# Optimization experiments

Hardware: AMD Instinct MI355X
Metric: run time of the kernel (lower is better)

The kernel has to match this reference:

```python
import jax, jax.numpy as jnp
import numpy as np

B, C, T = 2, 2, 4
N_SRC = 49152   # npix at level 6 (12 * 4^6)
N_TGT = 12288   # npix at level 5 (12 * 4^5)
D = 128


def setup_inputs() -> dict:
    key = jax.random.key(0)
    k1, k2, k3, k4 = jax.random.split(key, 4)
    x = jax.random.normal(k1, (B, C, T, N_SRC, D), dtype=jnp.float32)
    parent_map = jax.random.randint(k2, (N_SRC,), 0, N_TGT)
    W = jax.random.normal(k3, (D, D), dtype=jnp.float32) * 0.05  # Conv1d kernel_size=1 weight [out,in]
    b = jax.random.normal(k4, (D,), dtype=jnp.float32) * 0.05    # Conv1d bias
    return {"x": x, "parent_map": parent_map, "W": W, "b": b}


def reference(x, parent_map, W, b):
    # HEALPix downsample: scatter-add mean pooling over parent_map, then 1x1 conv.
    Bs, Cs, Ts, N, Dd = x.shape
    # flatten (b c t) and put pixel axis first for segment_sum: [N, BCT, D]
    x2 = x.reshape(Bs * Cs * Ts, N, Dd).transpose(1, 0, 2)
    sums = jax.ops.segment_sum(x2, parent_map, num_segments=N_TGT)          # [N_TGT, BCT, D]
    cnt = jax.ops.segment_sum(jnp.ones((N,), x.dtype), parent_map, num_segments=N_TGT)
    mean = sums / jnp.clip(cnt, 1e-6)[:, None, None]
    # 1x1 Conv1d over channel dim D: y = W @ mean + b
    out = jnp.einsum('mbd,ed->mbe', mean, W) + b                            # [N_TGT, BCT, D]
    return out.transpose(1, 0, 2).reshape(Bs, Cs, Ts, N_TGT, Dd)
```

## Files before the change

### kernel.cpp

```cpp
#include <hip/hip_runtime.h>
#include <stdint.h>

#define NSRC 49152
#define NTGT 12288
#define DIM  128
#define MPER 8
#define ROWS (MPER*16)
#define CAP  32
#define OSTR 132

using short8  = __attribute__((ext_vector_type(8))) short;
using short4v = __attribute__((ext_vector_type(4))) short;
using bf16x8  = __attribute__((ext_vector_type(8))) __bf16;
using f32x4   = __attribute__((ext_vector_type(4))) float;

__device__ __forceinline__ short f2bf(float f){
  unsigned int u = __float_as_uint(f);
  return (short)((u + 0x7fffu + ((u >> 16) & 1u)) >> 16);
}

__global__ void k_setup(const int* __restrict__ pm,
                        int* __restrict__ counts, int* __restrict__ child,
                        const float* __restrict__ W, short* __restrict__ Wt){
  const int b = blockIdx.x;
  if (b < 192){
    int i = b * 256 + threadIdx.x;
    int p = pm[i];
    int pos = atomicAdd(&counts[p], 1);
    if (pos < CAP) child[p * CAP + pos] = i;
  } else {
    int t  = (b - 192) * 256 + threadIdx.x;
    int e  = t & 127;
    int kk = t >> 7;
    const float4* src = (const float4*)(W + (size_t)e * DIM + kk * 8);
    float4 u = src[0], v = src[1];
    short8 h;
    h[0]=f2bf(u.x); h[1]=f2bf(u.y); h[2]=f2bf(u.z); h[3]=f2bf(u.w);
    h[4]=f2bf(v.x); h[5]=f2bf(v.y); h[6]=f2bf(v.z); h[7]=f2bf(v.w);
    *reinterpret_cast<short8*>(Wt + ((size_t)kk * 128 + e) * 8) = h;
  }
}

__global__ __launch_bounds__(256, 4) void k_fused(
    const float* __restrict__ x, const short* __restrict__ Wt,
    const float* __restrict__ bias,
    const int* __restrict__ counts, const int* __restrict__ child,
    float* __restrict__ out)
{
  __shared__ __align__(16) char smem[64 * OSTR * 4];
  short* s_mean = (short*)smem;
  float* s_out  = (float*)smem;
  const int tid = threadIdx.x;
  const int m0  = blockIdx.x * MPER;

  {
    const int o = tid & 7;
    #pragma unroll
    for (int it = 0; it < 4; ++it){
      const int r   = it * 32 + (tid >> 3);
      const int m   = m0 + (r >> 4);
      const int bct = r & 15;
      int cnt = counts[m]; cnt = (cnt > CAP) ? CAP : cnt;
      const int* cl = child + (size_t)m * CAP;
      const float* rowb = x + (size_t)bct * NSRC * DIM;
      float4 acc[4];
      #pragma unroll
      for (int s = 0; s < 4; ++s) acc[s] = make_float4(0.f, 0.f, 0.f, 0.f);
      int c = 0;
      for (; c + 1 < cnt; c += 2){
        const int n0 = cl[c], n1 = cl[c + 1];
        const float4* p0 = (const float4*)(rowb + (size_t)n0 * DIM) + o;
        const float4* p1 = (const float4*)(rowb + (size_t)n1 * DIM) + o;
        float4 v0[4], v1[4];
        #pragma unroll
        for (int s = 0; s < 4; ++s) v0[s] = p0[s * 8];
        #pragma unroll
        for (int s = 0; s < 4; ++s) v1[s] = p1[s * 8];
        #pragma unroll
        for (int s = 0; s < 4; ++s){
          acc[s].x += v0[s].x + v1[s].x; acc[s].y += v0[s].y + v1[s].y;
          acc[s].z += v0[s].z + v1[s].z; acc[s].w += v0[s].w + v1[s].w;
        }
      }
      if (c < cnt){
        const int n0 = cl[c];
        const float4* p0 = (const float4*)(rowb + (size_t)n0 * DIM) + o;
        #pragma unroll
        for (int s = 0; s < 4; ++s){
          float4 v = p0[s * 8];
          acc[s].x += v.x; acc[s].y += v.y; acc[s].z += v.z; acc[s].w += v.w;
        }
      }
      const float inv = (cnt > 0) ? (1.0f / (float)cnt) : 0.0f;
      const int rsw = (r & 7) << 3;
      #pragma unroll
      for (int s = 0; s < 4; ++s){
        const int col = s * 32 + o * 4;
        short4v h;
        h[0] = f2bf(acc[s].x * inv); h[1] = f2bf(acc[s].y * inv);
        h[2] = f2bf(acc[s].z * inv); h[3] = f2bf(acc[s].w * inv);
        *reinterpret_cast<short4v*>(&s_mean[r * DIM + (col ^ rsw)]) = h;
      }
    }
  }

  __syncthreads();

  const int w  = tid >> 6;
  const int l  = tid & 63;
  const int lr = l & 15;
  const int kg = l >> 4;
  f32x4 acc[2][8];
  #pragma unroll
  for (int i = 0; i < 2; ++i)
    #pragma unroll
    for (int n = 0; n < 8; ++n) acc[i][n] = (f32x4){0.f, 0.f, 0.f, 0.f};

  #pragma unroll 1
  for (int ks = 0; ks < 4; ++ks){
    const int k = ks * 32 + kg * 8;
    bf16x8 af[2];
    #pragma unroll
    for (int i = 0; i < 2; ++i){
      const int row = w * 32 + i * 16 + lr;
      af[i] = *reinterpret_cast<bf16x8*>(&s_mean[row * DIM + (k ^ ((row & 7) << 3))]);
    }
    const short* wp = Wt + ((size_t)(ks * 4 + kg) * 128 + lr) * 8;
    #pragma unroll
    for (int n = 0; n < 8; ++n){
      bf16x8 bfr = *reinterpret_cast<const bf16x8*>(wp + n * 128);
      acc[0][n] = __builtin_amdgcn_mfma_f32_16x16x32_bf16(af[0], bfr, acc[0][n], 0, 0, 0);
      acc[1][n] = __builtin_amdgcn_mfma_f32_16x16x32_bf16(af[1], bfr, acc[1][n], 0, 0, 0);
    }
  }

  float bv[8];
  #pragma unroll
  for (int n = 0; n < 8; ++n) bv[n] = bias[n * 16 + lr];

  #pragma unroll
  for (int round = 0; round < 2; ++round){
    __syncthreads();
    if ((w >> 1) == round){
      #pragma unroll
      for (int i = 0; i < 2; ++i)
        #pragma unroll
        for (int j = 0; j < 4; ++j){
          const int grl = (w & 1) * 32 + i * 16 + (l >> 4) * 4 + j;
          #pragma unroll
          for (int n = 0; n < 8; ++n)
            s_out[grl * OSTR + n * 16 + lr] = acc[i][n][j] + bv[n];
        }
    }
    __syncthreads();
    #pragma unroll
    for (int r2 = 0; r2 < 4; ++r2){
      const int bct = w * 4 + r2;
      #pragma unroll
      for (int it2 = 0; it2 < 2; ++it2){
        const int f  = it2 * 64 + l;
        const int mi = f >> 5, d4 = f & 31;
        f32x4 v = *reinterpret_cast<f32x4*>(&s_out[(mi * 16 + bct) * OSTR + d4 * 4]);
        float* gp = out + ((size_t)bct * NTGT + m0 + round * 4 + mi) * DIM + d4 * 4;
        __builtin_nontemporal_store(v, reinterpret_cast<f32x4*>(gp));
      }
    }
  }
}

extern "C" void kernel_launch(void* const* d_in, const int* in_sizes, int n_in,
                              void* d_out, int out_size, void* d_ws, size_t ws_size,
                              hipStream_t stream) {
  const float* x    = (const float*)d_in[0];
  const int*   pm   = (const int*)  d_in[1];
  const float* W    = (const float*)d_in[2];
  const float* bias = (const float*)d_in[3];
  float* out = (float*)d_out;

  int*   counts = (int*)d_ws;
  int*   child  = counts + NTGT;
  short* Wt     = (short*)(child + NTGT * CAP);

  hipMemsetAsync(counts, 0, NTGT * sizeof(int), stream);
  k_setup<<<200, 256, 0, stream>>>(pm, counts, child, W, Wt);
  k_fused<<<NTGT/MPER, 256, 0, stream>>>(x, Wt, bias, counts, child, out);
}
```

Before: 123.9 us.

## Halve targets per block, prefetch child indices, use nontemporal gather loads

Cuts the number of target pixels per block from 8 to 4, so the grid doubles and each wave handles one 16-row MFMA tile, and the output staging collapses to a single round. The child-index list is prefetched as two int4 loads and the gather is unrolled up to 8 children, with nontemporal loads on the streaming x reads. The aim is more blocks in flight to hide gather latency and fewer serialized LDS rounds. In exchange, each Wt fragment is reused by fewer rows, and each block does less work against the same per-block fixed overhead.

```diff
diff --git a/kernel.cpp b/kernel.cpp
--- a/kernel.cpp
+++ b/kernel.cpp
@@ -4,7 +4,7 @@
 #define NSRC 49152
 #define NTGT 12288
 #define DIM  128
-#define MPER 8
+#define MPER 4
 #define ROWS (MPER*16)
 #define CAP  32
 #define OSTR 132
@@ -47,58 +47,61 @@
     const int* __restrict__ counts, const int* __restrict__ child,
     float* __restrict__ out)
 {
-  __shared__ __align__(16) char smem[64 * OSTR * 4];
+  __shared__ __align__(16) char smem[ROWS * OSTR * 4];
   short* s_mean = (short*)smem;
   float* s_out  = (float*)smem;
   const int tid = threadIdx.x;
   const int m0  = blockIdx.x * MPER;
 
   {
-    const int o = tid & 7;
+    const int o  = tid & 7;
+    const int rr = tid >> 3;
     #pragma unroll
-    for (int it = 0; it < 4; ++it){
-      const int r   = it * 32 + (tid >> 3);
+    for (int it = 0; it < 2; ++it){
+      const int r   = it * 32 + rr;
       const int m   = m0 + (r >> 4);
       const int bct = r & 15;
       int cnt = counts[m]; cnt = (cnt > CAP) ? CAP : cnt;
       const int* cl = child + (size_t)m * CAP;
+      const int4 i03 = *reinterpret_cast<const int4*>(cl);
+      const int4 i47 = *reinterpret_cast<const int4*>(cl + 4);
       const float* rowb = x + (size_t)bct * NSRC * DIM;
-      float4 acc[4];
+      f32x4 acc[4];
       #pragma unroll
-      for (int s = 0; s < 4; ++s) acc[s] = make_float4(0.f, 0.f, 0.f, 0.f);
-      int c = 0;
-      for (; c + 1 < cnt; c += 2){
-        const int n0 = cl[c], n1 = cl[c + 1];
-        const float4* p0 = (const float4*)(rowb + (size_t)n0 * DIM) + o;
-        const float4* p1 = (const float4*)(rowb + (size_t)n1 * DIM) + o;
-        float4 v0[4], v1[4];
+      for (int s = 0; s < 4; ++s) acc[s] = (f32x4){0.f, 0.f, 0.f, 0.f};
+
+      auto G2 = [&](int n0, int n1){
+        const f32x4* p0 = (const f32x4*)(rowb + (size_t)n0 * DIM) + o;
+        const f32x4* p1 = (const f32x4*)(rowb + (size_t)n1 * DIM) + o;
+        f32x4 v0[4], v1[4];
         #pragma unroll
-        for (int s = 0; s < 4; ++s) v0[s] = p0[s * 8];
+        for (int s = 0; s < 4; ++s) v0[s] = __builtin_nontemporal_load(p0 + s * 8);
         #pragma unroll
-        for (int s = 0; s < 4; ++s) v1[s] = p1[s * 8];
+        for (int s = 0; s < 4; ++s) v1[s] = __builtin_nontemporal_load(p1 + s * 8);
         #pragma unroll
-        for (int s = 0; s < 4; ++s){
-          acc[s].x += v0[s].x + v1[s].x; acc[s].y += v0[s].y + v1[s].y;
-          acc[s].z += v0[s].z + v1[s].z; acc[s].w += v0[s].w + v1[s].w;
-        }
-      }
-      if (c < cnt){
-        const int n0 = cl[c];
-        const float4* p0 = (const float4*)(rowb + (size_t)n0 * DIM) + o;
+        for (int s = 0; s < 4; ++s) acc[s] += v0[s] + v1[s];
+      };
+      auto G1 = [&](int n0){
+        const f32x4* p0 = (const f32x4*)(rowb + (size_t)n0 * DIM) + o;
         #pragma unroll
-        for (int s = 0; s < 4; ++s){
-          float4 v = p0[s * 8];
-          acc[s].x += v.x; acc[s].y += v.y; acc[s].z += v.z; acc[s].w += v.w;
-        }
-      }
+        for (int s = 0; s < 4; ++s) acc[s] += __builtin_nontemporal_load(p0 + s * 8);
+      };
+
+      if (cnt > 1) G2(i03.x, i03.y);
+      if (cnt > 3) G2(i03.z, i03.w);
+      if (cnt > 5) G2(i47.x, i47.y);
+      if (cnt > 7) G2(i47.z, i47.w);
+      int c = (cnt < 8) ? (cnt & ~1) : 8;
+      for (; c < cnt; ++c) G1(cl[c]);
+
       const float inv = (cnt > 0) ? (1.0f / (float)cnt) : 0.0f;
       const int rsw = (r & 7) << 3;
       #pragma unroll
       for (int s = 0; s < 4; ++s){
         const int col = s * 32 + o * 4;
         short4v h;
-        h[0] = f2bf(acc[s].x * inv); h[1] = f2bf(acc[s].y * inv);
-        h[2] = f2bf(acc[s].z * inv); h[3] = f2bf(acc[s].w * inv);
+        h[0] = f2bf(acc[s][0] * inv); h[1] = f2bf(acc[s][1] * inv);
+        h[2] = f2bf(acc[s][2] * inv); h[3] = f2bf(acc[s][3] * inv);
         *reinterpret_cast<short4v*>(&s_mean[r * DIM + (col ^ rsw)]) = h;
       }
     }
@@ -110,27 +113,20 @@
   const int l  = tid & 63;
   const int lr = l & 15;
   const int kg = l >> 4;
-  f32x4 acc[2][8];
+  f32x4 acc[8];
   #pragma unroll
-  for (int i = 0; i < 2; ++i)
-    #pragma unroll
-    for (int n = 0; n < 8; ++n) acc[i][n] = (f32x4){0.f, 0.f, 0.f, 0.f};
+  for (int n = 0; n < 8; ++n) acc[n] = (f32x4){0.f, 0.f, 0.f, 0.f};
 
   #pragma unroll 1
   for (int ks = 0; ks < 4; ++ks){
     const int k = ks * 32 + kg * 8;
-    bf16x8 af[2];
-    #pragma unroll
-    for (int i = 0; i < 2; ++i){
-      const int row = w * 32 + i * 16 + lr;
-      af[i] = *reinterpret_cast<bf16x8*>(&s_mean[row * DIM + (k ^ ((row & 7) << 3))]);
-    }
+    const int row = w * 16 + lr;
+    bf16x8 af = *reinterpret_cast<bf16x8*>(&s_mean[row * DIM + (k ^ ((row & 7) << 3))]);
     const short* wp = Wt + ((size_t)(ks * 4 + kg) * 128 + lr) * 8;
     #pragma unroll
     for (int n = 0; n < 8; ++n){
       bf16x8 bfr = *reinterpret_cast<const bf16x8*>(wp + n * 128);
-      acc[0][n] = __builtin_amdgcn_mfma_f32_16x16x32_bf16(af[0], bfr, acc[0][n], 0, 0, 0);
-      acc[1][n] = __builtin_amdgcn_mfma_f32_16x16x32_bf16(af[1], bfr, acc[1][n], 0, 0, 0);
+      acc[n] = __builtin_amdgcn_mfma_f32_16x16x32_bf16(af, bfr, acc[n], 0, 0, 0);
     }
   }
 
@@ -138,32 +134,25 @@
   #pragma unroll
   for (int n = 0; n < 8; ++n) bv[n] = bias[n * 16 + lr];
 
+  __syncthreads();
   #pragma unroll
-  for (int round = 0; round < 2; ++round){
-    __syncthreads();
-    if ((w >> 1) == round){
-      #pragma unroll
-      for (int i = 0; i < 2; ++i)
-        #pragma unroll
-        for (int j = 0; j < 4; ++j){
-          const int grl = (w & 1) * 32 + i * 16 + (l >> 4) * 4 + j;
-          #pragma unroll
-          for (int n = 0; n < 8; ++n)
-            s_out[grl * OSTR + n * 16 + lr] = acc[i][n][j] + bv[n];
-        }
-    }
-    __syncthreads();
+  for (int j = 0; j < 4; ++j){
+    const int grl = w * 16 + (l >> 4) * 4 + j;
     #pragma unroll
-    for (int r2 = 0; r2 < 4; ++r2){
-      const int bct = w * 4 + r2;
-      #pragma unroll
-      for (int it2 = 0; it2 < 2; ++it2){
-        const int f  = it2 * 64 + l;
-        const int mi = f >> 5, d4 = f & 31;
-        f32x4 v = *reinterpret_cast<f32x4*>(&s_out[(mi * 16 + bct) * OSTR + d4 * 4]);
-        float* gp = out + ((size_t)bct * NTGT + m0 + round * 4 + mi) * DIM + d4 * 4;
-        __builtin_nontemporal_store(v, reinterpret_cast<f32x4*>(gp));
-      }
+    for (int n = 0; n < 8; ++n)
+      s_out[grl * OSTR + n * 16 + lr] = acc[n][j] + bv[n];
+  }
+  __syncthreads();
+  #pragma unroll
+  for (int r2 = 0; r2 < 4; ++r2){
+    const int bct = w * 4 + r2;
+    #pragma unroll
+    for (int it2 = 0; it2 < 2; ++it2){
+      const int f  = it2 * 64 + l;
+      const int mi = f >> 5, d4 = f & 31;
+      f32x4 v = *reinterpret_cast<f32x4*>(&s_out[(mi * 16 + bct) * OSTR + d4 * 4]);
+      float* gp = out + ((size_t)bct * NTGT + m0 + mi) * DIM + d4 * 4;
+      __builtin_nontemporal_store(v, reinterpret_cast<f32x4*>(gp));
     }
   }
 }
```

Result: faster. 115.5 us (-6.8%).
